# Optimization experiments

Hardware: AMD Instinct MI355X
Metric: run time of the kernel (lower is better)

Reference implementation:

```python
import jax, jax.numpy as jnp
import numpy as np

B, T, C = 2, 2048, 1024
H = 16
HD = C // H  # head_dim = 64
SCALE = HD ** -0.5

def setup_inputs() -> dict:
    key = jax.random.key(0)
    ks = jax.random.split(key, 5)
    s = 1.0 / np.sqrt(C)
    return {
        "x": jax.random.normal(ks[0], (B, T, C), dtype=jnp.float32),
        "Wq": jax.random.normal(ks[1], (C, C), dtype=jnp.float32) * s,
        "Wk": jax.random.normal(ks[2], (C, C), dtype=jnp.float32) * s,
        "Wv": jax.random.normal(ks[3], (C, C), dtype=jnp.float32) * s,
        "Wp": jax.random.normal(ks[4], (C, C), dtype=jnp.float32) * s,
        "bp": jnp.zeros((C,), dtype=jnp.float32),
    }

def reference(x, Wq, Wk, Wv, Wp, bp):
    b, t, c = x.shape
    # QKV projections (no bias, qkv_bias=False) -> [B,T,H,HD]
    q = (x @ Wq).reshape(b, t, H, HD)
    k = (x @ Wk).reshape(b, t, H, HD)
    v = (x @ Wv).reshape(b, t, H, HD)
    # scores [B,H,T,T]
    scores = jnp.einsum("bqhd,bkhd->bhqk", q, k) * SCALE
    causal = jnp.tril(jnp.ones((t, t), dtype=bool))
    scores = jnp.where(causal, scores, -jnp.inf)
    attn = jax.nn.softmax(scores, axis=-1)  # dropout = identity (eval mode)
    out = jnp.einsum("bhqk,bkhd->bqhd", attn, v).reshape(b, t, c)
    return out @ Wp + bp
```

## Files before the change

### kernel.cpp

```cpp
#include <hip/hip_runtime.h>


typedef __attribute__((ext_vector_type(8))) short shortx8;
typedef __attribute__((ext_vector_type(4))) short shortx4;
typedef __attribute__((ext_vector_type(8))) unsigned short ushortx8;
typedef __attribute__((ext_vector_type(4))) float f32x4;
typedef __attribute__((ext_vector_type(16))) float f32x16;

#define MFMA16(a, b, c) __builtin_amdgcn_mfma_f32_16x16x32_bf16((a), (b), (c), 0, 0, 0)
#define MFMA32(a, b, c) __builtin_amdgcn_mfma_f32_32x32x16_bf16((a), (b), (c), 0, 0, 0)

#define SC_L2E 0.18033688011112042f

__device__ __forceinline__ unsigned short f2bf(float f) {
  union { float f; unsigned u; } v; v.f = f;
  unsigned r = v.u + 0x7fffu + ((v.u >> 16) & 1u);
  return (unsigned short)(r >> 16);
}

__device__ __forceinline__ float fexp2(float x) {
#if __has_builtin(__builtin_amdgcn_exp2f)
  return __builtin_amdgcn_exp2f(x);
#else
  return exp2f(x);
#endif
}

__device__ __forceinline__ void gload16(const void* g, void* l) {
  __builtin_amdgcn_global_load_lds(
      (const __attribute__((address_space(1))) void*)g,
      (__attribute__((address_space(3))) void*)l, 16, 0, 0);
}

__global__ __launch_bounds__(256) void cvt_x(const float* __restrict__ x,
                                             unsigned short* __restrict__ xb, int n4) {
  int i = blockIdx.x * 256 + threadIdx.x;
  if (i < n4) {
    float4 v = ((const float4*)x)[i];
    unsigned short* o = xb + (size_t)i * 4;
    o[0] = f2bf(v.x); o[1] = f2bf(v.y); o[2] = f2bf(v.z); o[3] = f2bf(v.w);
  }
}

__global__ __launch_bounds__(256) void transpose_w4(
    const float* __restrict__ Wq, const float* __restrict__ Wk,
    const float* __restrict__ Wv, const float* __restrict__ Wp,
    unsigned short* __restrict__ wqkvT, unsigned short* __restrict__ wpT) {
  __shared__ float tile[32][33];
  const int zi = blockIdx.z;
  const float* src = (zi == 0) ? Wq : (zi == 1) ? Wk : (zi == 2) ? Wv : Wp;
  unsigned short* dst = (zi == 3) ? wpT : wqkvT + (size_t)zi * 1048576;
  const int bx = blockIdx.x * 32, by = blockIdx.y * 32;
  const int tx = threadIdx.x & 31, ty = threadIdx.x >> 5;
  #pragma unroll
  for (int i = 0; i < 32; i += 8)
    tile[ty + i][tx] = src[(size_t)(by + ty + i) * 1024 + bx + tx];
  __syncthreads();
  #pragma unroll
  for (int i = 0; i < 32; i += 8)
    dst[(size_t)(bx + ty + i) * 1024 + by + tx] = f2bf(tile[tx][ty + i]);
}

__global__ __launch_bounds__(256) void gemm_bt(
    const unsigned short* __restrict__ A, const unsigned short* __restrict__ BT,
    unsigned short* __restrict__ Cb, float* __restrict__ Cf,
    const float* __restrict__ bias, int M, int N, int K,
    float qscale, int scale_cols, unsigned short* __restrict__ vTo) {
  __shared__ unsigned short As[128 * 32];
  __shared__ unsigned short Bs[128 * 32];
  const int tid = threadIdx.x;
  const int lane = tid & 63, w = tid >> 6;
  const int wr = w >> 1, wc = w & 1;
  const int brow = blockIdx.y << 7, bcol = blockIdx.x << 7;

  f32x4 z = {0.f, 0.f, 0.f, 0.f};
  f32x4 acc[4][4];
  #pragma unroll
  for (int m = 0; m < 4; ++m)
    #pragma unroll
    for (int n = 0; n < 4; ++n) acc[m][n] = z;

  const int srow = tid >> 2;
  const int scol = (tid & 3) << 3;
  const unsigned short* Ap = A + (size_t)(brow + srow) * K + scol;
  const unsigned short* Bp = BT + (size_t)(bcol + srow) * K + scol;
  unsigned short* AsW = &As[w * 512];
  unsigned short* BsW = &Bs[w * 512];
  const size_t rowK64 = (size_t)64 * K;

  for (int k0 = 0; k0 < K; k0 += 32) {
    gload16(Ap + k0, AsW);
    gload16(Ap + rowK64 + k0, AsW + 2048);
    gload16(Bp + k0, BsW);
    gload16(Bp + rowK64 + k0, BsW + 2048);
    __syncthreads();
    shortx8 af[4], bf[4];
    const int koff = (lane >> 4) << 3;
    const int ar = (wr << 6) + (lane & 15);
    const int br = (wc << 6) + (lane & 15);
    #pragma unroll
    for (int m = 0; m < 4; ++m) af[m] = *(const shortx8*)&As[(ar + m * 16) * 32 + koff];
    #pragma unroll
    for (int n = 0; n < 4; ++n) bf[n] = *(const shortx8*)&Bs[(br + n * 16) * 32 + koff];
    #pragma unroll
    for (int m = 0; m < 4; ++m)
      #pragma unroll
      for (int n = 0; n < 4; ++n) acc[m][n] = MFMA16(af[m], bf[n], acc[m][n]);
    __syncthreads();
  }

  const int r0 = (lane >> 4) << 2;
  const int c0 = lane & 15;
  if (Cb) {
    if (vTo && bcol >= 2048) {
      #pragma unroll
      for (int m = 0; m < 4; ++m)
        #pragma unroll
        for (int n = 0; n < 4; ++n) {
          const int dp = bcol - 2048 + (wc << 6) + n * 16 + c0;
          const size_t rowb = brow + (wr << 6) + m * 16 + r0;
          shortx4 o4;
          #pragma unroll
          for (int j = 0; j < 4; ++j) o4[j] = (short)f2bf(acc[m][n][j]);
          *(shortx4*)&vTo[(size_t)dp * 4096 + rowb] = o4;
        }
    } else {
      #pragma unroll
      for (int m = 0; m < 4; ++m)
        #pragma unroll
        for (int n = 0; n < 4; ++n)
          #pragma unroll
          for (int j = 0; j < 4; ++j) {
            const size_t row = brow + (wr << 6) + m * 16 + r0 + j;
            const size_t col = bcol + (wc << 6) + n * 16 + c0;
            float v = acc[m][n][j];
            if ((int)col < scale_cols) v *= qscale;
            Cb[row * N + col] = f2bf(v);
          }
    }
  } else {
    #pragma unroll
    for (int m = 0; m < 4; ++m)
      #pragma unroll
      for (int n = 0; n < 4; ++n)
        #pragma unroll
        for (int j = 0; j < 4; ++j) {
          const size_t row = brow + (wr << 6) + m * 16 + r0 + j;
          const size_t col = bcol + (wc << 6) + n * 16 + c0;
          Cf[row * N + col] = acc[m][n][j] + bias[col];
        }
  }
}


__global__ __launch_bounds__(128, 4) void attn_fwd(
    const unsigned short* __restrict__ qkv, const unsigned short* __restrict__ vT,
    unsigned short* __restrict__ att) {
  __shared__ unsigned short sh[2][4096];

  const int tid = threadIdx.x;
  const int lane = tid & 63;
  const int p = tid >> 6;
  const int stream = blockIdx.x;
  const int h = stream & 15, b = stream >> 4;
  const int qb = 63 - (int)blockIdx.y;
  const int ql = lane & 31;
  const int hi = lane >> 5;
  const int q = qb * 32 + ql;

  shortx8 qf[4];
  {
    const unsigned short* qp = qkv + ((size_t)(b * 2048 + q)) * 3072 + h * 64 + 8 * hi;
    #pragma unroll
    for (int kc = 0; kc < 4; ++kc) qf[kc] = *(const shortx8*)(qp + 16 * kc);
  }

  f32x16 z16;
  #pragma unroll
  for (int i = 0; i < 16; ++i) z16[i] = 0.f;
  f32x16 accO0 = z16, accO1 = z16;
  float m_run = -__builtin_inff(), l_run = 0.f;

  const unsigned short* kb[4];
  const unsigned short* vb[4];
  #pragma unroll
  for (int i = 0; i < 4; ++i) {
    const int krow = 8 * i + (lane >> 3);
    const int kcl = (lane & 7) ^ (((krow >> 1) ^ (krow >> 4)) & 7);
    kb[i] = qkv + ((size_t)(b * 2048 + krow)) * 3072 + 1024 + h * 64 + 8 * kcl;
    const int vrow = 16 * i + (lane >> 2);
    const int vcl = (lane & 3) ^ (((vrow >> 1) ^ (vrow >> 3)) & 3);
    vb[i] = vT + ((size_t)(h * 64 + vrow)) * 4096 + b * 2048 + 8 * vcl;
  }
  const int rs8 = ((ql >> 1) ^ (ql >> 4)) & 7;
  const int rs4 = ((ql >> 1) ^ (ql >> 3)) & 3;

  unsigned short* Kl = &sh[p][0];
  unsigned short* Vl = &sh[p][2048];

  #define STAGE(t_)                                                        \
    do {                                                                   \
      _Pragma("unroll")                                                    \
      for (int i = 0; i < 4; ++i) {                                        \
        gload16(kb[i] + (size_t)(t_) * 32 * 3072, Kl + i * 512);           \
        gload16(vb[i] + (t_) * 32, Vl + i * 512);                          \
      }                                                                    \
    } while (0)

  if (p <= qb) STAGE(p);
  for (int t = p; t <= qb; t += 2) {
    asm volatile("s_waitcnt vmcnt(0)" ::: "memory");
    __builtin_amdgcn_sched_barrier(0);

    shortx8 kf[4];
    #pragma unroll
    for (int kc = 0; kc < 4; ++kc)
      kf[kc] = *(const shortx8*)&Kl[ql * 64 + 8 * ((2 * kc + hi) ^ rs8)];
    shortx8 vf[2][2];
    #pragma unroll
    for (int dh = 0; dh < 2; ++dh)
      #pragma unroll
      for (int ks = 0; ks < 2; ++ks)
        vf[dh][ks] = *(const shortx8*)&Vl[(32 * dh + ql) * 32 + 8 * ((2 * ks + hi) ^ rs4)];
    asm volatile("s_waitcnt lgkmcnt(0)" ::: "memory");
    __builtin_amdgcn_sched_barrier(0);

    if (t + 2 <= qb) STAGE(t + 2);

    __builtin_amdgcn_s_setprio(1);
    f32x16 s = z16;
    #pragma unroll
    for (int kc = 0; kc < 4; ++kc) s = MFMA32(kf[kc], qf[kc], s);
    __builtin_amdgcn_s_setprio(0);

    if (t == qb) {
      #pragma unroll
      for (int r = 0; r < 16; ++r) {
        const int kvl = (r & 3) + 8 * (r >> 2) + 4 * hi;
        if (kvl > ql) s[r] = -__builtin_inff();
      }
    }

    float m8[8], m4[4];
    #pragma unroll
    for (int i = 0; i < 8; ++i) m8[i] = fmaxf(s[2 * i], s[2 * i + 1]);
    #pragma unroll
    for (int i = 0; i < 4; ++i) m4[i] = fmaxf(m8[2 * i], m8[2 * i + 1]);
    float mx = fmaxf(fmaxf(m4[0], m4[1]), fmaxf(m4[2], m4[3]));
    mx = fmaxf(mx, __shfl_xor(mx, 32));

    if (!__all(mx <= m_run + 8.0f)) {
      const float nm = fmaxf(m_run, mx);
      const float alpha = fexp2(m_run - nm);
      l_run *= alpha;
      #pragma unroll
      for (int r = 0; r < 16; ++r) { accO0[r] *= alpha; accO1[r] *= alpha; }
      m_run = nm;
    }

    #pragma unroll
    for (int r = 0; r < 16; ++r) s[r] = fexp2(s[r] - m_run);
    float a8[8], a4[4];
    #pragma unroll
    for (int i = 0; i < 8; ++i) a8[i] = s[2 * i] + s[2 * i + 1];
    #pragma unroll
    for (int i = 0; i < 4; ++i) a4[i] = a8[2 * i] + a8[2 * i + 1];
    float rsum = (a4[0] + a4[1]) + (a4[2] + a4[3]);
    rsum += __shfl_xor(rsum, 32);
    l_run += rsum;

    unsigned wv[8], xv[8];
    #pragma unroll
    for (int i = 0; i < 8; ++i)
      asm("v_cvt_pk_bf16_f32 %0, %1, %2" : "=v"(wv[i]) : "v"(s[2 * i]), "v"(s[2 * i + 1]));
    #pragma unroll
    for (int i = 0; i < 8; ++i) xv[i] = __shfl_xor(wv[i], 32);
    __builtin_amdgcn_s_setprio(1);
    #pragma unroll
    for (int ss = 0; ss < 2; ++ss) {
      union { unsigned u[4]; shortx8 s8; } pb;
      pb.u[0] = hi ? xv[4 * ss + 2] : wv[4 * ss];
      pb.u[1] = hi ? xv[4 * ss + 3] : wv[4 * ss + 1];
      pb.u[2] = hi ? wv[4 * ss + 2] : xv[4 * ss];
      pb.u[3] = hi ? wv[4 * ss + 3] : xv[4 * ss + 1];
      accO0 = MFMA32(vf[0][ss], pb.s8, accO0);
      accO1 = MFMA32(vf[1][ss], pb.s8, accO1);
    }
    __builtin_amdgcn_s_setprio(0);
  }
  #undef STAGE

  __syncthreads();
  float* mb = (float*)&sh[0][0];
  float* ml = mb + 2048;
  if (p == 1) {
    #pragma unroll
    for (int rg = 0; rg < 4; ++rg) {
      f32x4 v0 = {accO0[4 * rg], accO0[4 * rg + 1], accO0[4 * rg + 2], accO0[4 * rg + 3]};
      f32x4 v1 = {accO1[4 * rg], accO1[4 * rg + 1], accO1[4 * rg + 2], accO1[4 * rg + 3]};
      *(f32x4*)&mb[(rg * 64 + lane) * 4] = v0;
      *(f32x4*)&mb[((4 + rg) * 64 + lane) * 4] = v1;
    }
    ml[lane] = m_run;
    ml[64 + lane] = l_run;
  }
  __syncthreads();
  if (p == 0) {
    const float m1 = ml[lane], l1 = ml[64 + lane];
    const float mf = fmaxf(m_run, m1);
    const float a0 = fexp2(m_run - mf);
    const float a1 = fexp2(m1 - mf);
    const float inv = 1.f / (l_run * a0 + l1 * a1);
    unsigned short* op = att + ((size_t)(b * 2048 + q)) * 1024 + h * 64;
    #pragma unroll
    for (int rq = 0; rq < 4; ++rq) {
      f32x4 p0 = *(const f32x4*)&mb[(rq * 64 + lane) * 4];
      f32x4 p1 = *(const f32x4*)&mb[((4 + rq) * 64 + lane) * 4];
      shortx4 o0, o1;
      #pragma unroll
      for (int j = 0; j < 4; ++j) {
        o0[j] = (short)f2bf((accO0[4 * rq + j] * a0 + p0[j] * a1) * inv);
        o1[j] = (short)f2bf((accO1[4 * rq + j] * a0 + p1[j] * a1) * inv);
      }
      *(shortx4*)&op[8 * rq + 4 * hi] = o0;
      *(shortx4*)&op[32 + 8 * rq + 4 * hi] = o1;
    }
  }
}

extern "C" void kernel_launch(void* const* d_in, const int* in_sizes, int n_in,
                              void* d_out, int out_size, void* d_ws, size_t ws_size,
                              hipStream_t stream) {
  const float* x  = (const float*)d_in[0];
  const float* Wq = (const float*)d_in[1];
  const float* Wk = (const float*)d_in[2];
  const float* Wv = (const float*)d_in[3];
  const float* Wp = (const float*)d_in[4];
  const float* bp = (const float*)d_in[5];

  char* ws = (char*)d_ws;
  unsigned short* xb    = (unsigned short*)(ws);
  unsigned short* wqkvT = (unsigned short*)(ws + (size_t)8  * 1048576);
  unsigned short* wpT   = (unsigned short*)(ws + (size_t)14 * 1048576);
  unsigned short* qkv   = (unsigned short*)(ws + (size_t)16 * 1048576);
  unsigned short* vT    = (unsigned short*)(ws + (size_t)40 * 1048576);
  unsigned short* att   = (unsigned short*)(ws + (size_t)48 * 1048576);

  cvt_x<<<dim3(4096), dim3(256), 0, stream>>>(x, xb, 1048576);
  transpose_w4<<<dim3(32, 32, 4), dim3(256), 0, stream>>>(Wq, Wk, Wv, Wp, wqkvT, wpT);
  gemm_bt<<<dim3(24, 32), dim3(256), 0, stream>>>(xb, wqkvT, qkv, nullptr, nullptr,
                                                  4096, 3072, 1024, SC_L2E, 1024, vT);
  attn_fwd<<<dim3(32, 64), dim3(128), 0, stream>>>(qkv, vT, att);
  gemm_bt<<<dim3(8, 32), dim3(256), 0, stream>>>(att, wpT, nullptr, (float*)d_out, bp,
                                                 4096, 1024, 1024, 0.f, 0, nullptr);
}
```

Before: 124.8 us.

## Swizzle GEMM LDS tiles and transpose MFMA output for vectorized epilogue stores

```diff
diff --git a/kernel.cpp b/kernel.cpp
--- a/kernel.cpp
+++ b/kernel.cpp
@@ -16,6 +16,12 @@
   union { float f; unsigned u; } v; v.f = f;
   unsigned r = v.u + 0x7fffu + ((v.u >> 16) & 1u);
   return (unsigned short)(r >> 16);
+}
+
+__device__ __forceinline__ unsigned cvtpk(float a, float b) {
+  unsigned r;
+  asm("v_cvt_pk_bf16_f32 %0, %1, %2" : "=v"(r) : "v"(a), "v"(b));
+  return r;
 }
 
 __device__ __forceinline__ float fexp2(float x) {
@@ -72,6 +78,7 @@
   const int lane = tid & 63, w = tid >> 6;
   const int wr = w >> 1, wc = w & 1;
   const int brow = blockIdx.y << 7, bcol = blockIdx.x << 7;
+  const bool vpath = (vTo != nullptr) && (bcol >= 2048);
 
   f32x4 z = {0.f, 0.f, 0.f, 0.f};
   f32x4 acc[4][4];
@@ -81,12 +88,16 @@
     for (int n = 0; n < 4; ++n) acc[m][n] = z;
 
   const int srow = tid >> 2;
-  const int scol = (tid & 3) << 3;
+  const int scol = (((tid & 3) ^ (srow & 3)) << 3);
   const unsigned short* Ap = A + (size_t)(brow + srow) * K + scol;
   const unsigned short* Bp = BT + (size_t)(bcol + srow) * K + scol;
   unsigned short* AsW = &As[w * 512];
   unsigned short* BsW = &Bs[w * 512];
   const size_t rowK64 = (size_t)64 * K;
+
+  const int fsw = ((lane >> 4) ^ (lane & 3)) << 3;
+  const int ar = (wr << 6) + (lane & 15);
+  const int br = (wc << 6) + (lane & 15);
 
   for (int k0 = 0; k0 < K; k0 += 32) {
     gload16(Ap + k0, AsW);
@@ -95,60 +106,74 @@
     gload16(Bp + rowK64 + k0, BsW + 2048);
     __syncthreads();
     shortx8 af[4], bf[4];
-    const int koff = (lane >> 4) << 3;
-    const int ar = (wr << 6) + (lane & 15);
-    const int br = (wc << 6) + (lane & 15);
-    #pragma unroll
-    for (int m = 0; m < 4; ++m) af[m] = *(const shortx8*)&As[(ar + m * 16) * 32 + koff];
-    #pragma unroll
-    for (int n = 0; n < 4; ++n) bf[n] = *(const shortx8*)&Bs[(br + n * 16) * 32 + koff];
-    #pragma unroll
-    for (int m = 0; m < 4; ++m)
-      #pragma unroll
-      for (int n = 0; n < 4; ++n) acc[m][n] = MFMA16(af[m], bf[n], acc[m][n]);
-    __syncthreads();
-  }
-
-  const int r0 = (lane >> 4) << 2;
-  const int c0 = lane & 15;
-  if (Cb) {
-    if (vTo && bcol >= 2048) {
+    #pragma unroll
+    for (int m = 0; m < 4; ++m) af[m] = *(const shortx8*)&As[(ar + m * 16) * 32 + fsw];
+    #pragma unroll
+    for (int n = 0; n < 4; ++n) bf[n] = *(const shortx8*)&Bs[(br + n * 16) * 32 + fsw];
+    if (vpath) {
       #pragma unroll
       for (int m = 0; m < 4; ++m)
         #pragma unroll
-        for (int n = 0; n < 4; ++n) {
-          const int dp = bcol - 2048 + (wc << 6) + n * 16 + c0;
-          const size_t rowb = brow + (wr << 6) + m * 16 + r0;
-          shortx4 o4;
-          #pragma unroll
-          for (int j = 0; j < 4; ++j) o4[j] = (short)f2bf(acc[m][n][j]);
-          *(shortx4*)&vTo[(size_t)dp * 4096 + rowb] = o4;
-        }
+        for (int n = 0; n < 4; ++n) acc[m][n] = MFMA16(af[m], bf[n], acc[m][n]);
     } else {
       #pragma unroll
       for (int m = 0; m < 4; ++m)
         #pragma unroll
-        for (int n = 0; n < 4; ++n)
-          #pragma unroll
-          for (int j = 0; j < 4; ++j) {
-            const size_t row = brow + (wr << 6) + m * 16 + r0 + j;
-            const size_t col = bcol + (wc << 6) + n * 16 + c0;
-            float v = acc[m][n][j];
-            if ((int)col < scale_cols) v *= qscale;
-            Cb[row * N + col] = f2bf(v);
-          }
-    }
+        for (int n = 0; n < 4; ++n) acc[m][n] = MFMA16(bf[n], af[m], acc[m][n]);
+    }
+    __syncthreads();
+  }
+
+  if (vpath) {
+    const int r0 = (lane >> 4) << 2;
+    const int c0 = lane & 15;
+    #pragma unroll
+    for (int m = 0; m < 4; ++m)
+      #pragma unroll
+      for (int n = 0; n < 4; ++n) {
+        const int dp = bcol - 2048 + (wc << 6) + n * 16 + c0;
+        const size_t rowb = brow + (wr << 6) + m * 16 + r0;
+        uint2 u;
+        u.x = cvtpk(acc[m][n][0], acc[m][n][1]);
+        u.y = cvtpk(acc[m][n][2], acc[m][n][3]);
+        *(uint2*)&vTo[(size_t)dp * 4096 + rowb] = u;
+      }
   } else {
-    #pragma unroll
-    for (int m = 0; m < 4; ++m)
-      #pragma unroll
-      for (int n = 0; n < 4; ++n)
+    const int c0 = lane & 15;
+    const int r0 = (lane >> 4) << 2;
+    if (Cb) {
+      #pragma unroll
+      for (int m = 0; m < 4; ++m) {
+        const size_t row = brow + (wr << 6) + m * 16 + c0;
         #pragma unroll
-        for (int j = 0; j < 4; ++j) {
-          const size_t row = brow + (wr << 6) + m * 16 + r0 + j;
-          const size_t col = bcol + (wc << 6) + n * 16 + c0;
-          Cf[row * N + col] = acc[m][n][j] + bias[col];
+        for (int n = 0; n < 4; ++n) {
+          const int colb = bcol + (wc << 6) + n * 16 + r0;
+          float v0 = acc[m][n][0], v1 = acc[m][n][1];
+          float v2 = acc[m][n][2], v3 = acc[m][n][3];
+          if (colb < scale_cols) { v0 *= qscale; v1 *= qscale; v2 *= qscale; v3 *= qscale; }
+          uint2 u;
+          u.x = cvtpk(v0, v1);
+          u.y = cvtpk(v2, v3);
+          *(uint2*)&Cb[row * N + colb] = u;
         }
+      }
+    } else {
+      #pragma unroll
+      for (int m = 0; m < 4; ++m) {
+        const size_t row = brow + (wr << 6) + m * 16 + c0;
+        #pragma unroll
+        for (int n = 0; n < 4; ++n) {
+          const int colb = bcol + (wc << 6) + n * 16 + r0;
+          const float4 b4 = *(const float4*)&bias[colb];
+          float4 o;
+          o.x = acc[m][n][0] + b4.x;
+          o.y = acc[m][n][1] + b4.y;
+          o.z = acc[m][n][2] + b4.z;
+          o.w = acc[m][n][3] + b4.w;
+          *(float4*)&Cf[row * N + colb] = o;
+        }
+      }
+    }
   }
 }
 
@@ -271,8 +296,7 @@
 
     unsigned wv[8], xv[8];
     #pragma unroll
-    for (int i = 0; i < 8; ++i)
-      asm("v_cvt_pk_bf16_f32 %0, %1, %2" : "=v"(wv[i]) : "v"(s[2 * i]), "v"(s[2 * i + 1]));
+    for (int i = 0; i < 8; ++i) wv[i] = cvtpk(s[2 * i], s[2 * i + 1]);
     #pragma unroll
     for (int i = 0; i < 8; ++i) xv[i] = __shfl_xor(wv[i], 32);
     __builtin_amdgcn_s_setprio(1);
```

New measurement: 153.2 us. 1.23x slower.
